# Kernel tuning notes

Hardware: AMD Instinct MI355X
Metric: run time of the kernel (lower is better)

The kernel has to match this reference:

```python
import jax, jax.numpy as jnp
import numpy as np

IMG_H = 256; IMG_W = 256; N_PTS = 192
MIN_DEPTH = 3.0; MAX_DEPTH = 9.0
NDC_EXTENT = 1.0; FOCAL = 4.0  # focal length so rays at volume center span ~[-1,1]
EPS = 1e-8; EA_EPS = 1e-10


def setup_inputs() -> dict:
    key = jax.random.key(0)
    image3d = jax.random.uniform(key, (1, 1, 128, 128, 128), dtype=jnp.float32)
    R = jnp.eye(3, dtype=jnp.float32)[None]            # [1,3,3] camera rotation
    T = jnp.array([[0.0, 0.0, 4.0]], dtype=jnp.float32)  # camera center at world (0,0,-4)
    return {"image3d": image3d, "R": R, "T": T}


def _trilinear(vol, pts):
    # vol: [C,D,H,W]; pts: [N,3] xyz in [-1,1]; align_corners=True, zero padding
    C, D, H, W = vol.shape
    fx = (pts[:, 0] + 1.0) * 0.5 * (W - 1)
    fy = (pts[:, 1] + 1.0) * 0.5 * (H - 1)
    fz = (pts[:, 2] + 1.0) * 0.5 * (D - 1)
    x0 = jnp.floor(fx); y0 = jnp.floor(fy); z0 = jnp.floor(fz)
    wx = fx - x0; wy = fy - y0; wz = fz - z0
    out = jnp.zeros((pts.shape[0], C), vol.dtype)
    for dz in (0, 1):
        for dy in (0, 1):
            for dx in (0, 1):
                xi = x0 + dx; yi = y0 + dy; zi = z0 + dz
                w = ((wx if dx else 1.0 - wx) * (wy if dy else 1.0 - wy)
                     * (wz if dz else 1.0 - wz))
                valid = ((xi >= 0) & (xi <= W - 1) & (yi >= 0) & (yi <= H - 1)
                         & (zi >= 0) & (zi <= D - 1))
                xc = jnp.clip(xi, 0, W - 1).astype(jnp.int32)
                yc = jnp.clip(yi, 0, H - 1).astype(jnp.int32)
                zc = jnp.clip(zi, 0, D - 1).astype(jnp.int32)
                vals = vol[:, zc, yc, xc]          # [C,N] gather
                out = out + (w * valid).astype(vol.dtype)[:, None] * vals.T
    return out                                      # [N,C]


def reference(image3d, R, T):
    B = image3d.shape[0]
    features = jnp.repeat(image3d, 3, axis=1)                 # [B,3,D,H,W]
    densities = jnp.ones_like(image3d) / N_PTS                # [B,1,D,H,W]
    vol4 = jnp.concatenate([features, densities], axis=1)     # [B,4,D,H,W]
    # NDC pixel grid + depths along each ray
    ys = jnp.linspace(1.0, -1.0, IMG_H)
    xs = jnp.linspace(1.0, -1.0, IMG_W)
    yg, xg = jnp.meshgrid(ys, xs, indexing="ij")              # [H,W]
    depths = jnp.linspace(MIN_DEPTH, MAX_DEPTH, N_PTS)        # [P]
    x_cam = xg[..., None] * depths / FOCAL                    # [H,W,P]
    y_cam = yg[..., None] * depths / FOCAL
    z_cam = jnp.broadcast_to(depths, x_cam.shape)
    pts_cam = jnp.stack([x_cam, y_cam, z_cam], axis=-1)       # [H,W,P,3]
    # X_cam = X_world @ R + T  =>  X_world = (X_cam - T) @ R^T
    pts_world = jnp.einsum("bhwpj,bij->bhwpi",
                           pts_cam[None] - T[:, None, None, None, :], R)
    local = pts_world / NDC_EXTENT                            # volume local coords in [-1,1]
    sampled = jax.vmap(_trilinear)(vol4, local.reshape(B, -1, 3))  # [B,N,4]
    sampled = sampled.reshape(B, IMG_H, IMG_W, N_PTS, 4)
    feats = sampled[..., :3]
    dens = sampled[..., 3]                                    # [B,H,W,P]
    # EmissionAbsorption raymarcher (shifted cumprod of transmittance)
    t = (1.0 + EA_EPS) - dens
    cp = jnp.cumprod(t, axis=-1)
    absorption = jnp.concatenate([jnp.ones_like(cp[..., :1]), cp[..., :-1]], axis=-1)
    weights = dens * absorption
    rgb = jnp.einsum("bhwp,bhwpc->bhwc", weights, feats)      # [B,H,W,3]
    opac = 1.0 - jnp.prod(1.0 - dens, axis=-1, keepdims=True)
    rgba = jnp.concatenate([rgb, opac], axis=-1)              # [B,H,W,4]
    screen = jnp.transpose(rgba, (0, 3, 1, 2))                # [B,4,H,W]
    gray = screen.mean(axis=1, keepdims=True)                 # [B,1,H,W]
    # normalized(standardized(x))  (torch std is unbiased -> ddof=1)
    std = (gray - gray.mean()) / (jnp.std(gray, ddof=1) + EPS)
    out = (std - std.min() + EPS) / (std.max() - std.min() + EPS)
    return out
```

## Files before the change

kernel.cpp:

```cpp
#include <hip/hip_runtime.h>
#include <math.h>

#define N_PIX (256 * 256)
#define N_PTS 192
#define SEGS 8
#define TILE_PIX 64
#define N_BLK (N_PIX / TILE_PIX)
#define THREADS (TILE_PIX * SEGS)

__global__ __launch_bounds__(THREADS) void render_kernel(
    const float* __restrict__ vol,
    const float* __restrict__ Rm,
    const float* __restrict__ Tv,
    float* __restrict__ out,
    float* __restrict__ part)
{
    const int tid = threadIdx.x;
    const int seg = tid >> 6;
    const int l   = tid & 63;
    const int tr  = blockIdx.x >> 5;
    const int tc  = blockIdx.x & 31;
    const int h = tr * 8 + (l >> 3);
    const int w = tc * 8 + (l & 7);
    const float yg = 1.0f - (2.0f / 255.0f) * (float)h;
    const float xg = 1.0f - (2.0f / 255.0f) * (float)w;

    const float r00 = Rm[0], r01 = Rm[1], r02 = Rm[2];
    const float r10 = Rm[3], r11 = Rm[4], r12 = Rm[5];
    const float r20 = Rm[6], r21 = Rm[7], r22 = Rm[8];
    const float t0 = Tv[0], t1 = Tv[1], t2 = Tv[2];

    const float a0 = 0.25f * (r00 * xg + r01 * yg) + r02;
    const float a1 = 0.25f * (r10 * xg + r11 * yg) + r12;
    const float a2 = 0.25f * (r20 * xg + r21 * yg) + r22;
    const float b0 = -(r00 * t0 + r01 * t1 + r02 * t2);
    const float b1 = -(r10 * t0 + r11 * t1 + r12 * t2);
    const float b2 = -(r20 * t0 + r21 * t1 + r22 * t2);

    const float LIM = 1.0f + 2.0f / 127.0f + 1e-4f;
    float dlo = 3.0f, dhi = 9.0f;
    {
        const float aa[3] = {a0, a1, a2};
        const float bb[3] = {b0, b1, b2};
        #pragma unroll
        for (int k = 0; k < 3; ++k) {
            const float a = aa[k], b = bb[k];
            if (fabsf(a) > 1e-12f) {
                const float i0 = (-LIM - b) / a;
                const float i1 = ( LIM - b) / a;
                dlo = fmaxf(dlo, fminf(i0, i1));
                dhi = fminf(dhi, fmaxf(i0, i1));
            } else if (fabsf(b) >= LIM) {
                dhi = -1e30f;
            }
        }
    }
    const float step = 6.0f / 191.0f;
    const float rstep = 191.0f / 6.0f;
    int plo = (int)ceilf((dlo - 3.0f) * rstep - 1e-3f);
    int phi = (int)floorf((dhi - 3.0f) * rstep + 1e-3f);
    plo = max(plo, 0);
    phi = min(phi, N_PTS - 1);
    int len = phi - plo + 1;
    if (len < 0) len = 0;
    const int chunk = (len + SEGS - 1) >> 3;
    const int iBeg = plo + seg * chunk;
    const int iEnd = min(iBeg + chunk, plo + len);

    float P = 1.0f;
    float U = 1.0f;
    float S = 0.0f;

    #pragma unroll 2
    for (int p = iBeg; p < iEnd; ++p) {
        const float d = fmaf(step, (float)p, 3.0f);
        const float fx = (fmaf(a0, d, b0) + 1.0f) * 63.5f;
        const float fy = (fmaf(a1, d, b1) + 1.0f) * 63.5f;
        const float fz = (fmaf(a2, d, b2) + 1.0f) * 63.5f;
        const float x0f = floorf(fx), y0f = floorf(fy), z0f = floorf(fz);
        const float wx = fx - x0f, wy = fy - y0f, wz = fz - z0f;
        const int ix = (int)x0f, iy = (int)y0f, iz = (int)z0f;
        const float ax0 = (ix >= 0  && ix <= 127) ? (1.0f - wx) : 0.0f;
        const float ax1 = (ix >= -1 && ix <= 126) ? wx : 0.0f;
        const float ay0 = (iy >= 0  && iy <= 127) ? (1.0f - wy) : 0.0f;
        const float ay1 = (iy >= -1 && iy <= 126) ? wy : 0.0f;
        const float az0 = (iz >= 0  && iz <= 127) ? (1.0f - wz) : 0.0f;
        const float az1 = (iz >= -1 && iz <= 126) ? wz : 0.0f;
        const float s = (ax0 + ax1) * (ay0 + ay1) * (az0 + az1);
        const float dens = s * (1.0f / 192.0f);
        const int xc0 = min(max(ix, 0), 127);
        const int xc1 = min(max(ix + 1, 0), 127);
        const int yc0 = min(max(iy, 0), 127);
        const int yc1 = min(max(iy + 1, 0), 127);
        const int zc0 = min(max(iz, 0), 127);
        const int zc1 = min(max(iz + 1, 0), 127);
        const float* q00 = vol + (zc0 * 128 + yc0) * 128;
        const float* q01 = vol + (zc0 * 128 + yc1) * 128;
        const float* q10 = vol + (zc1 * 128 + yc0) * 128;
        const float* q11 = vol + (zc1 * 128 + yc1) * 128;
        const float v000 = q00[xc0], v001 = q00[xc1];
        const float v010 = q01[xc0], v011 = q01[xc1];
        const float v100 = q10[xc0], v101 = q10[xc1];
        const float v110 = q11[xc0], v111 = q11[xc1];
        const float feat =
            az0 * (ay0 * (ax0 * v000 + ax1 * v001) + ay1 * (ax0 * v010 + ax1 * v011)) +
            az1 * (ay0 * (ax0 * v100 + ax1 * v101) + ay1 * (ax0 * v110 + ax1 * v111));
        S = fmaf(dens * P, feat, S);
        P *= (1.0f + 1e-10f - dens);
        U *= (1.0f - dens);
    }

    __shared__ float sP[SEGS][TILE_PIX];
    __shared__ float sU[SEGS][TILE_PIX];
    __shared__ float sS[SEGS][TILE_PIX];
    sP[seg][l] = P;
    sU[seg][l] = U;
    sS[seg][l] = S;
    __syncthreads();

    if (tid < TILE_PIX) {
        float absorb = 1.0f, uAll = 1.0f, wS = 0.0f;
        #pragma unroll
        for (int s = 0; s < SEGS; ++s) {
            wS = fmaf(absorb, sS[s][l], wS);
            absorb *= sP[s][l];
            uAll   *= sU[s][l];
        }
        const float g = (3.0f * wS + (1.0f - uAll)) * 0.25f;
        out[h * 256 + w] = g;

        float vs = g, vq = g * g, vmn = g, vmx = g;
        #pragma unroll
        for (int off = 1; off < 64; off <<= 1) {
            vs += __shfl_xor(vs, off);
            vq += __shfl_xor(vq, off);
            vmn = fminf(vmn, __shfl_xor(vmn, off));
            vmx = fmaxf(vmx, __shfl_xor(vmx, off));
        }
        if (l == 0) {
            part[blockIdx.x]             = vs;
            part[N_BLK + blockIdx.x]     = vq;
            part[2 * N_BLK + blockIdx.x] = vmn;
            part[3 * N_BLK + blockIdx.x] = vmx;
        }
    }
}

__global__ __launch_bounds__(256) void finish_kernel(
    float* __restrict__ out,
    const float* __restrict__ part)
{
    const int tid = threadIdx.x;
    __shared__ float s_s[4], s_q[4], s_n[4], s_x[4];
    __shared__ float s_fin[4];

    float fs  = part[tid]               + part[tid + 256]
              + part[tid + 512]         + part[tid + 768];
    float fq  = part[N_BLK + tid]       + part[N_BLK + tid + 256]
              + part[N_BLK + tid + 512] + part[N_BLK + tid + 768];
    float fn  = fminf(fminf(part[2 * N_BLK + tid],       part[2 * N_BLK + tid + 256]),
                      fminf(part[2 * N_BLK + tid + 512], part[2 * N_BLK + tid + 768]));
    float fx2 = fmaxf(fmaxf(part[3 * N_BLK + tid],       part[3 * N_BLK + tid + 256]),
                      fmaxf(part[3 * N_BLK + tid + 512], part[3 * N_BLK + tid + 768]));
    #pragma unroll
    for (int off = 1; off < 64; off <<= 1) {
        fs += __shfl_xor(fs, off);
        fq += __shfl_xor(fq, off);
        fn  = fminf(fn,  __shfl_xor(fn, off));
        fx2 = fmaxf(fx2, __shfl_xor(fx2, off));
    }
    const int wave = tid >> 6;
    const int lane = tid & 63;
    if (lane == 0) { s_s[wave] = fs; s_q[wave] = fq; s_n[wave] = fn; s_x[wave] = fx2; }
    __syncthreads();
    if (tid == 0) {
        const float tsum = s_s[0] + s_s[1] + s_s[2] + s_s[3];
        const float tsq  = s_q[0] + s_q[1] + s_q[2] + s_q[3];
        const float tmn  = fminf(fminf(s_n[0], s_n[1]), fminf(s_n[2], s_n[3]));
        const float tmx  = fmaxf(fmaxf(s_x[0], s_x[1]), fmaxf(s_x[2], s_x[3]));
        const float N = (float)N_PIX;
        const float mean = tsum / N;
        float var = (tsq - N * mean * mean) / (N - 1.0f);
        if (var < 0.0f) var = 0.0f;
        const float denom = sqrtf(var) + 1e-8f;
        s_fin[0] = mean;
        s_fin[1] = denom;
        s_fin[2] = (tmn - mean) / denom;
        s_fin[3] = (tmx - mean) / denom;
    }
    __syncthreads();

    const float mean = s_fin[0];
    const float rdenom = 1.0f / s_fin[1];
    const float smin = s_fin[2];
    const float rrange = 1.0f / (s_fin[3] - smin + 1e-8f);
    const int i = blockIdx.x * 256 + tid;
    const float sv = (out[i] - mean) * rdenom;
    out[i] = (sv - smin + 1e-8f) * rrange;
}

extern "C" void kernel_launch(void* const* d_in, const int* in_sizes, int n_in,
                              void* d_out, int out_size, void* d_ws, size_t ws_size,
                              hipStream_t stream)
{
    const float* vol = (const float*)d_in[0];
    const float* Rm  = (const float*)d_in[1];
    const float* Tv  = (const float*)d_in[2];
    float* out = (float*)d_out;
    float* part = (float*)d_ws;

    hipLaunchKernelGGL(render_kernel, dim3(N_BLK), dim3(THREADS), 0, stream,
                       vol, Rm, Tv, out, part);
    hipLaunchKernelGGL(finish_kernel, dim3(N_PIX / 256), dim3(256), 0, stream,
                       out, part);
}
```

Before: 88.42 us.

## Prepack volume into float4 xy-neighbor quads for two-load trilinear sampling

```diff
diff --git a/kernel.cpp b/kernel.cpp
--- a/kernel.cpp
+++ b/kernel.cpp
@@ -7,9 +7,23 @@
 #define TILE_PIX 64
 #define N_BLK (N_PIX / TILE_PIX)
 #define THREADS (TILE_PIX * SEGS)
+#define VOL4_ELEMS (128 * 128 * 128)
+
+__global__ __launch_bounds__(256) void pack_kernel(
+    const float* __restrict__ vol, float4* __restrict__ vol4)
+{
+    const int idx = blockIdx.x * 256 + threadIdx.x;
+    const int x = idx & 127;
+    const int y = (idx >> 7) & 127;
+    const int z = idx >> 14;
+    const int x1 = min(x + 1, 127);
+    const float* row0 = vol + (z * 128 + y) * 128;
+    const float* row1 = vol + (z * 128 + min(y + 1, 127)) * 128;
+    vol4[idx] = make_float4(row0[x], row0[x1], row1[x], row1[x1]);
+}
 
 __global__ __launch_bounds__(THREADS) void render_kernel(
-    const float* __restrict__ vol,
+    const float4* __restrict__ vol4,
     const float* __restrict__ Rm,
     const float* __restrict__ Tv,
     float* __restrict__ out,
@@ -88,23 +102,22 @@
         const float az1 = (iz >= -1 && iz <= 126) ? wz : 0.0f;
         const float s = (ax0 + ax1) * (ay0 + ay1) * (az0 + az1);
         const float dens = s * (1.0f / 192.0f);
-        const int xc0 = min(max(ix, 0), 127);
-        const int xc1 = min(max(ix + 1, 0), 127);
-        const int yc0 = min(max(iy, 0), 127);
-        const int yc1 = min(max(iy + 1, 0), 127);
+
+        int xi = ix; float wx0 = ax0, wx1 = ax1;
+        if (xi < 0) { xi = 0; wx0 = ax1; wx1 = 0.0f; } else { xi = min(xi, 127); }
+        int yi = iy; float wy0 = ay0, wy1 = ay1;
+        if (yi < 0) { yi = 0; wy0 = ay1; wy1 = 0.0f; } else { yi = min(yi, 127); }
         const int zc0 = min(max(iz, 0), 127);
         const int zc1 = min(max(iz + 1, 0), 127);
-        const float* q00 = vol + (zc0 * 128 + yc0) * 128;
-        const float* q01 = vol + (zc0 * 128 + yc1) * 128;
-        const float* q10 = vol + (zc1 * 128 + yc0) * 128;
-        const float* q11 = vol + (zc1 * 128 + yc1) * 128;
-        const float v000 = q00[xc0], v001 = q00[xc1];
-        const float v010 = q01[xc0], v011 = q01[xc1];
-        const float v100 = q10[xc0], v101 = q10[xc1];
-        const float v110 = q11[xc0], v111 = q11[xc1];
-        const float feat =
-            az0 * (ay0 * (ax0 * v000 + ax1 * v001) + ay1 * (ax0 * v010 + ax1 * v011)) +
-            az1 * (ay0 * (ax0 * v100 + ax1 * v101) + ay1 * (ax0 * v110 + ax1 * v111));
+
+        const float4 c0 = vol4[(zc0 * 128 + yi) * 128 + xi];
+        const float4 c1 = vol4[(zc1 * 128 + yi) * 128 + xi];
+        const float bil0 = wy0 * (wx0 * c0.x + wx1 * c0.y)
+                         + wy1 * (wx0 * c0.z + wx1 * c0.w);
+        const float bil1 = wy0 * (wx0 * c1.x + wx1 * c1.y)
+                         + wy1 * (wx0 * c1.z + wx1 * c1.w);
+        const float feat = az0 * bil0 + az1 * bil1;
+
         S = fmaf(dens * P, feat, S);
         P *= (1.0f + 1e-10f - dens);
         U *= (1.0f - dens);
@@ -207,10 +220,13 @@
     const float* Rm  = (const float*)d_in[1];
     const float* Tv  = (const float*)d_in[2];
     float* out = (float*)d_out;
-    float* part = (float*)d_ws;
-
+    float4* vol4 = (float4*)d_ws;
+    float* part = (float*)d_ws + 4 * VOL4_ELEMS;
+
+    hipLaunchKernelGGL(pack_kernel, dim3(VOL4_ELEMS / 256), dim3(256), 0, stream,
+                       vol, vol4);
     hipLaunchKernelGGL(render_kernel, dim3(N_BLK), dim3(THREADS), 0, stream,
-                       vol, Rm, Tv, out, part);
+                       vol4, Rm, Tv, out, part);
     hipLaunchKernelGGL(finish_kernel, dim3(N_PIX / 256), dim3(256), 0, stream,
                        out, part);
 }
```

After: 85.74 us. -3.0%, faster.

## Split rays into interior fast path with constant density and closed-form transmittance

Applied to the files above, without the earlier changes.

```diff
diff --git a/kernel.cpp b/kernel.cpp
--- a/kernel.cpp
+++ b/kernel.cpp
@@ -7,6 +7,44 @@
 #define TILE_PIX 64
 #define N_BLK (N_PIX / TILE_PIX)
 #define THREADS (TILE_PIX * SEGS)
+
+#define L2Q  (-0.0075336725f)
+#define QF   (0.99479166677f)
+
+__device__ __forceinline__ void general_step(
+    const float* __restrict__ vol, float pf,
+    float A0, float B0, float A1, float B1, float A2, float B2,
+    float& S, float& Prun)
+{
+    const float fx = fmaf(A0, pf, B0);
+    const float fy = fmaf(A1, pf, B1);
+    const float fz = fmaf(A2, pf, B2);
+    const float x0f = floorf(fx), y0f = floorf(fy), z0f = floorf(fz);
+    const float wx = fx - x0f, wy = fy - y0f, wz = fz - z0f;
+    const int ix = (int)x0f, iy = (int)y0f, iz = (int)z0f;
+    const float ax0 = (ix >= 0  && ix <= 127) ? (1.0f - wx) : 0.0f;
+    const float ax1 = (ix >= -1 && ix <= 126) ? wx : 0.0f;
+    const float ay0 = (iy >= 0  && iy <= 127) ? (1.0f - wy) : 0.0f;
+    const float ay1 = (iy >= -1 && iy <= 126) ? wy : 0.0f;
+    const float az0 = (iz >= 0  && iz <= 127) ? (1.0f - wz) : 0.0f;
+    const float az1 = (iz >= -1 && iz <= 126) ? wz : 0.0f;
+    const float s = (ax0 + ax1) * (ay0 + ay1) * (az0 + az1);
+    const float dens = s * (1.0f / 192.0f);
+    const int xc0 = min(max(ix, 0), 127), xc1 = min(max(ix + 1, 0), 127);
+    const int yc0 = min(max(iy, 0), 127), yc1 = min(max(iy + 1, 0), 127);
+    const int zc0 = min(max(iz, 0), 127), zc1 = min(max(iz + 1, 0), 127);
+    const float* q00 = vol + (zc0 * 128 + yc0) * 128;
+    const float* q01 = vol + (zc0 * 128 + yc1) * 128;
+    const float* q10 = vol + (zc1 * 128 + yc0) * 128;
+    const float* q11 = vol + (zc1 * 128 + yc1) * 128;
+    const float feat =
+        az0 * (ay0 * (ax0 * q00[xc0] + ax1 * q00[xc1]) +
+               ay1 * (ax0 * q01[xc0] + ax1 * q01[xc1])) +
+        az1 * (ay0 * (ax0 * q10[xc0] + ax1 * q10[xc1]) +
+               ay1 * (ax0 * q11[xc0] + ax1 * q11[xc1]));
+    S = fmaf(dens * Prun, feat, S);
+    Prun *= (1.0f + 1e-10f - dens);
+}
 
 __global__ __launch_bounds__(THREADS) void render_kernel(
     const float* __restrict__ vol,
@@ -37,8 +75,17 @@
     const float b1 = -(r10 * t0 + r11 * t1 + r12 * t2);
     const float b2 = -(r20 * t0 + r21 * t1 + r22 * t2);
 
+    const float step = 6.0f / 191.0f;
+    const float rstep = 191.0f / 6.0f;
+
+    const float A0 = a0 * step * 63.5f, B0 = (fmaf(a0, 3.0f, b0) + 1.0f) * 63.5f;
+    const float A1 = a1 * step * 63.5f, B1 = (fmaf(a1, 3.0f, b1) + 1.0f) * 63.5f;
+    const float A2 = a2 * step * 63.5f, B2 = (fmaf(a2, 3.0f, b2) + 1.0f) * 63.5f;
+
     const float LIM = 1.0f + 2.0f / 127.0f + 1e-4f;
+    const float WHI = 1.0f - 1e-5f;
     float dlo = 3.0f, dhi = 9.0f;
+    float dloI = 3.0f, dhiI = 9.0f;
     {
         const float aa[3] = {a0, a1, a2};
         const float bb[3] = {b0, b1, b2};
@@ -46,87 +93,93 @@
         for (int k = 0; k < 3; ++k) {
             const float a = aa[k], b = bb[k];
             if (fabsf(a) > 1e-12f) {
-                const float i0 = (-LIM - b) / a;
-                const float i1 = ( LIM - b) / a;
-                dlo = fmaxf(dlo, fminf(i0, i1));
-                dhi = fminf(dhi, fmaxf(i0, i1));
-            } else if (fabsf(b) >= LIM) {
-                dhi = -1e30f;
+                const float ra = 1.0f / a;
+                const float o0 = (-LIM - b) * ra, o1 = (LIM - b) * ra;
+                dlo = fmaxf(dlo, fminf(o0, o1));
+                dhi = fminf(dhi, fmaxf(o0, o1));
+                const float i0 = (-1.0f - b) * ra, i1 = (WHI - b) * ra;
+                dloI = fmaxf(dloI, fminf(i0, i1));
+                dhiI = fminf(dhiI, fmaxf(i0, i1));
+            } else {
+                if (fabsf(b) >= LIM) dhi = -1e30f;
+                if (b < -1.0f || b > WHI) dhiI = -1e30f;
             }
         }
     }
-    const float step = 6.0f / 191.0f;
-    const float rstep = 191.0f / 6.0f;
     int plo = (int)ceilf((dlo - 3.0f) * rstep - 1e-3f);
     int phi = (int)floorf((dhi - 3.0f) * rstep + 1e-3f);
     plo = max(plo, 0);
     phi = min(phi, N_PTS - 1);
     int len = phi - plo + 1;
-    if (len < 0) len = 0;
+    if (len < 0) { len = 0; phi = plo - 1; }
+    int plo2 = (int)ceilf((dloI - 3.0f) * rstep + 1e-3f);
+    int phi2 = (int)floorf((dhiI - 3.0f) * rstep - 1e-3f);
+    plo2 = max(plo2, plo);
+    phi2 = min(phi2, phi);
+    if (plo2 > phi2) { plo2 = phi + 1; phi2 = phi; }
+
     const int chunk = (len + SEGS - 1) >> 3;
-    const int iBeg = plo + seg * chunk;
-    const int iEnd = min(iBeg + chunk, plo + len);
-
-    float P = 1.0f;
-    float U = 1.0f;
+    const int beg = plo + seg * chunk;
+    const int end = min(beg + chunk, plo + len);
+
+    float Prun = 1.0f;
     float S = 0.0f;
 
-    #pragma unroll 2
-    for (int p = iBeg; p < iEnd; ++p) {
-        const float d = fmaf(step, (float)p, 3.0f);
-        const float fx = (fmaf(a0, d, b0) + 1.0f) * 63.5f;
-        const float fy = (fmaf(a1, d, b1) + 1.0f) * 63.5f;
-        const float fz = (fmaf(a2, d, b2) + 1.0f) * 63.5f;
+    const int aEnd = min(end, plo2);
+    for (int p = beg; p < aEnd; ++p)
+        general_step(vol, (float)p, A0, B0, A1, B1, A2, B2, S, Prun);
+
+    const int i0b = max(beg, plo2);
+    const int i1b = min(end, phi2 + 1);
+    float qp = 1.0f, S2 = 0.0f;
+    #pragma unroll 4
+    for (int p = i0b; p < i1b; ++p) {
+        const float pf = (float)p;
+        const float fx = fmaf(A0, pf, B0);
+        const float fy = fmaf(A1, pf, B1);
+        const float fz = fmaf(A2, pf, B2);
         const float x0f = floorf(fx), y0f = floorf(fy), z0f = floorf(fz);
         const float wx = fx - x0f, wy = fy - y0f, wz = fz - z0f;
         const int ix = (int)x0f, iy = (int)y0f, iz = (int)z0f;
-        const float ax0 = (ix >= 0  && ix <= 127) ? (1.0f - wx) : 0.0f;
-        const float ax1 = (ix >= -1 && ix <= 126) ? wx : 0.0f;
-        const float ay0 = (iy >= 0  && iy <= 127) ? (1.0f - wy) : 0.0f;
-        const float ay1 = (iy >= -1 && iy <= 126) ? wy : 0.0f;
-        const float az0 = (iz >= 0  && iz <= 127) ? (1.0f - wz) : 0.0f;
-        const float az1 = (iz >= -1 && iz <= 126) ? wz : 0.0f;
-        const float s = (ax0 + ax1) * (ay0 + ay1) * (az0 + az1);
-        const float dens = s * (1.0f / 192.0f);
-        const int xc0 = min(max(ix, 0), 127);
-        const int xc1 = min(max(ix + 1, 0), 127);
-        const int yc0 = min(max(iy, 0), 127);
-        const int yc1 = min(max(iy + 1, 0), 127);
-        const int zc0 = min(max(iz, 0), 127);
-        const int zc1 = min(max(iz + 1, 0), 127);
-        const float* q00 = vol + (zc0 * 128 + yc0) * 128;
-        const float* q01 = vol + (zc0 * 128 + yc1) * 128;
-        const float* q10 = vol + (zc1 * 128 + yc0) * 128;
-        const float* q11 = vol + (zc1 * 128 + yc1) * 128;
-        const float v000 = q00[xc0], v001 = q00[xc1];
-        const float v010 = q01[xc0], v011 = q01[xc1];
-        const float v100 = q10[xc0], v101 = q10[xc1];
-        const float v110 = q11[xc0], v111 = q11[xc1];
-        const float feat =
-            az0 * (ay0 * (ax0 * v000 + ax1 * v001) + ay1 * (ax0 * v010 + ax1 * v011)) +
-            az1 * (ay0 * (ax0 * v100 + ax1 * v101) + ay1 * (ax0 * v110 + ax1 * v111));
-        S = fmaf(dens * P, feat, S);
-        P *= (1.0f + 1e-10f - dens);
-        U *= (1.0f - dens);
-    }
+        const float* q0 = vol + ((iz * 128 + iy) * 128 + ix);
+        const float v000 = q0[0],     v001 = q0[1];
+        const float v010 = q0[128],   v011 = q0[129];
+        const float v100 = q0[16384], v101 = q0[16385];
+        const float v110 = q0[16512], v111 = q0[16513];
+        const float x00 = fmaf(wx, v001 - v000, v000);
+        const float x01 = fmaf(wx, v011 - v010, v010);
+        const float x10 = fmaf(wx, v101 - v100, v100);
+        const float x11 = fmaf(wx, v111 - v110, v110);
+        const float y0v = fmaf(wy, x01 - x00, x00);
+        const float y1v = fmaf(wy, x11 - x10, x10);
+        const float feat = fmaf(wz, y1v - y0v, y0v);
+        S2 = fmaf(qp, feat, S2);
+        qp *= QF;
+    }
+    if (i1b > i0b) {
+        const int kint = i1b - i0b;
+        S = fmaf(Prun * (1.0f / 192.0f), S2, S);
+        Prun *= exp2f((float)kint * L2Q);
+    }
+
+    const int bBeg = max(beg, phi2 + 1);
+    for (int p = bBeg; p < end; ++p)
+        general_step(vol, (float)p, A0, B0, A1, B1, A2, B2, S, Prun);
 
     __shared__ float sP[SEGS][TILE_PIX];
-    __shared__ float sU[SEGS][TILE_PIX];
     __shared__ float sS[SEGS][TILE_PIX];
-    sP[seg][l] = P;
-    sU[seg][l] = U;
+    sP[seg][l] = Prun;
     sS[seg][l] = S;
     __syncthreads();
 
     if (tid < TILE_PIX) {
-        float absorb = 1.0f, uAll = 1.0f, wS = 0.0f;
+        float absorb = 1.0f, wS = 0.0f;
         #pragma unroll
         for (int s = 0; s < SEGS; ++s) {
             wS = fmaf(absorb, sS[s][l], wS);
             absorb *= sP[s][l];
-            uAll   *= sU[s][l];
-        }
-        const float g = (3.0f * wS + (1.0f - uAll)) * 0.25f;
+        }
+        const float g = (3.0f * wS + (1.0f - absorb)) * 0.25f;
         out[h * 256 + w] = g;
 
         float vs = g, vq = g * g, vmn = g, vmx = g;
```

Result: faster. 78.34 us (-11.4%).
